# Kernel tuning notes

Hardware: AMD Instinct MI355X
Metric: run time of the kernel (lower is better)

Reference implementation:

```python
import jax, jax.numpy as jnp
import numpy as np

QD = 512        # query_dim == key_dim
SD = 64         # spa_embed_dim
K = 4           # num_attn heads
EPS = 1e-6      # LayerNorm eps (space2vec LayerNorm)
SLOPE = 0.01    # nn.LeakyReLU default negative_slope


def setup_inputs() -> dict:
    key = jax.random.key(0)
    ks = jax.random.split(key, 6)
    B, N = 4096, 32
    D = 2 * QD + SD  # concat dim when have_query_embed=True
    xav = (6.0 / (D + K)) ** 0.5
    return {
        "key_embeds": jax.random.normal(ks[0], (B, N, QD), dtype=jnp.float32),
        "key_spa_embeds": jax.random.normal(ks[1], (B, N, SD), dtype=jnp.float32),
        "query_embed": jax.random.normal(ks[2], (B, QD), dtype=jnp.float32),
        "atten_vecs": jax.random.uniform(ks[3], (D, K), minval=-xav, maxval=xav, dtype=jnp.float32),
        "post_w": jax.random.normal(ks[4], (QD, QD), dtype=jnp.float32) * 0.02,
        "post_b": jnp.zeros((QD,), dtype=jnp.float32),
        "pre_ln_g": jnp.ones((QD,), dtype=jnp.float32),
        "pre_ln_b": jnp.zeros((QD,), dtype=jnp.float32),
        "post_ln_g": jnp.ones((QD,), dtype=jnp.float32),
        "post_ln_b": jnp.zeros((QD,), dtype=jnp.float32),
    }


def _layernorm(x, g, b):
    m = jnp.mean(x, axis=-1, keepdims=True)
    v = jnp.mean((x - m) ** 2, axis=-1, keepdims=True)
    return g * (x - m) / jnp.sqrt(v + EPS) + b


def reference(key_embeds, key_spa_embeds, query_embed, atten_vecs,
              post_w, post_b, pre_ln_g, pre_ln_b, post_ln_g, post_ln_b):
    B, N, _ = key_embeds.shape
    # expand query over context points and concat: [B, N, 2*QD+SD]
    q_exp = jnp.broadcast_to(query_embed[:, None, :], (B, N, QD))
    concat = jnp.concatenate([q_exp, key_embeds, key_spa_embeds], axis=2)
    # attention logits per head: [B, N, K]
    attn = jnp.einsum('bnd,dk->bnk', concat, atten_vecs)
    attn = jax.nn.leaky_relu(attn, SLOPE)
    attn = jax.nn.softmax(attn, axis=1)  # softmax over context points
    # weighted sum per head, then average over heads: [B, QD]
    combined = jnp.einsum('bnk,bnd->bkd', attn, key_embeds).sum(axis=1) * (1.0 / K)
    combined = jax.nn.sigmoid(combined)
    # pre layernorm with residual from query
    combined = _layernorm(combined + query_embed, pre_ln_g, pre_ln_b)
    # post linear (dropout in eval mode = identity) + residual + post LN
    lin = combined @ post_w.T + post_b
    out = _layernorm(lin + combined, post_ln_g, post_ln_b)
    return out
```

## Files before the change

kernel.cpp:

```cpp
#include <hip/hip_runtime.h>
#include <hip/hip_bf16.h>

#define QD 512
#define SD 64
#define NCTX 32
#define KTOT 576
#define ROWB 1152

constexpr float EPS_LN = 1e-6f;
constexpr float SLOPE = 0.01f;

typedef __attribute__((ext_vector_type(8))) __bf16 bf16x8;
typedef __attribute__((ext_vector_type(4))) float f32x4;

__device__ __forceinline__ float red64(float v) {
#pragma unroll
    for (int m = 32; m; m >>= 1) v += __shfl_xor(v, m, 64);
    return v;
}

__device__ __forceinline__ float b2f(unsigned short u) {
    unsigned int x = ((unsigned int)u) << 16;
    return __builtin_bit_cast(float, x);
}

__device__ __forceinline__ int swz(int row, int off) {
    return row * ROWB + (off ^ ((row & 7) << 4));
}

__device__ __forceinline__ bf16x8 pack8(float4 a, float4 b) {
    bf16x8 r;
    r[0] = (__bf16)a.x; r[1] = (__bf16)a.y; r[2] = (__bf16)a.z; r[3] = (__bf16)a.w;
    r[4] = (__bf16)b.x; r[5] = (__bf16)b.y; r[6] = (__bf16)b.z; r[7] = (__bf16)b.w;
    return r;
}

__global__ __launch_bounds__(256, 3) void attn_fuse(
    const float* __restrict__ key, const float* __restrict__ spa,
    const float* __restrict__ query, const float* __restrict__ av,
    const float* __restrict__ lng, const float* __restrict__ lnb,
    float* __restrict__ yout)
{
    __shared__ __align__(16) unsigned char s_A[NCTX * ROWB];
    __shared__ __align__(16) unsigned char s_B[4 * ROWB];
    __shared__ float s_logit[NCTX][4];
    __shared__ float s_w[NCTX];
    __shared__ float s_red[8];
    __shared__ float s_ql[4];

    const int b = blockIdx.x;
    const int t = threadIdx.x;
    const int wave = t >> 6;
    const int lane = t & 63;

    const float* kb = key + (size_t)b * (NCTX * QD);
    const float* qb = query + (size_t)b * QD;
    const float* sb = spa + (size_t)b * (NCTX * SD);
    const float4* av4 = reinterpret_cast<const float4*>(av);

    float4 kreg[16];
#pragma unroll
    for (int i = 0; i < 8; ++i) {
        const float* krow = kb + (8 * wave + i) * QD;
        kreg[2 * i]     = reinterpret_cast<const float4*>(krow)[2 * lane];
        kreg[2 * i + 1] = reinterpret_cast<const float4*>(krow)[2 * lane + 1];
    }
    const int i2 = lane >> 3, j8 = lane & 7;
    const float* srow = sb + (8 * wave + i2) * SD + 8 * j8;
    const float4 sreg0 = reinterpret_cast<const float4*>(srow)[0];
    const float4 sreg1 = reinterpret_cast<const float4*>(srow)[1];
    float avreg[9];
#pragma unroll
    for (int r = 0; r < 9; ++r)
        avreg[r] = av[(size_t)(512 + lane * 9 + r) * 4 + wave];

#pragma unroll
    for (int i = 0; i < 8; ++i) {
        const int n = 8 * wave + i;
        *reinterpret_cast<bf16x8*>(&s_A[swz(n, 16 * lane)]) =
            pack8(kreg[2 * i], kreg[2 * i + 1]);
    }
    *reinterpret_cast<bf16x8*>(&s_A[swz(8 * wave + i2, 1024 + 16 * j8)]) =
        pack8(sreg0, sreg1);
#pragma unroll
    for (int r = 0; r < 9; ++r) {
        const int k = lane * 9 + r;
        *reinterpret_cast<__bf16*>(&s_B[wave * ROWB + ((2 * k) ^ (wave << 4))]) =
            (__bf16)avreg[r];
    }

    if (wave == 3) {
        const float4* q4 = reinterpret_cast<const float4*>(qb);
        float s0 = 0.f, s1 = 0.f, s2 = 0.f, s3 = 0.f;
#pragma unroll
        for (int h = 0; h < 2; ++h) {
            const float4 qv = q4[2 * lane + h];
            const float4 a0 = av4[8 * lane + 4 * h + 0];
            const float4 a1 = av4[8 * lane + 4 * h + 1];
            const float4 a2 = av4[8 * lane + 4 * h + 2];
            const float4 a3 = av4[8 * lane + 4 * h + 3];
            s0 += qv.x * a0.x + qv.y * a1.x + qv.z * a2.x + qv.w * a3.x;
            s1 += qv.x * a0.y + qv.y * a1.y + qv.z * a2.y + qv.w * a3.y;
            s2 += qv.x * a0.z + qv.y * a1.z + qv.z * a2.z + qv.w * a3.z;
            s3 += qv.x * a0.w + qv.y * a1.w + qv.z * a2.w + qv.w * a3.w;
        }
        s0 = red64(s0); s1 = red64(s1); s2 = red64(s2); s3 = red64(s3);
        if (lane == 0) { s_ql[0] = s0; s_ql[1] = s1; s_ql[2] = s2; s_ql[3] = s3; }
    }
    __syncthreads();

    if (wave < 2) {
        const int colB = lane & 15;
        const int kgrp = (lane >> 4) * 16;
        const int arow = 16 * wave + (lane & 15);
        f32x4 acc = {0.f, 0.f, 0.f, 0.f};
        bf16x8 bz;
#pragma unroll
        for (int e = 0; e < 8; ++e) bz[e] = (__bf16)0.0f;
#pragma unroll
        for (int ks = 0; ks < 18; ++ks) {
            const int koff = ks * 64 + kgrp;
            const bf16x8 af =
                *reinterpret_cast<const bf16x8*>(&s_A[swz(arow, koff)]);
            bf16x8 bf = bz;
            if (colB < 4)
                bf = *reinterpret_cast<const bf16x8*>(
                    &s_B[colB * ROWB + (koff ^ (colB << 4))]);
            acc = __builtin_amdgcn_mfma_f32_16x16x32_bf16(af, bf, acc, 0, 0, 0);
        }
        if (colB < 4) {
            const float qlk = s_ql[colB];
#pragma unroll
            for (int r = 0; r < 4; ++r) {
                const int row = 16 * wave + (lane >> 4) * 4 + r;
                float v = acc[r] + qlk;
                v = v > 0.f ? v : SLOPE * v;
                s_logit[row][colB] = v;
            }
        }
    }
    __syncthreads();

    if (wave == 0) {
        const int n = lane & 31;
        float v0 = s_logit[n][0], v1 = s_logit[n][1],
              v2 = s_logit[n][2], v3 = s_logit[n][3];
        float m0 = v0, m1 = v1, m2 = v2, m3 = v3;
#pragma unroll
        for (int m = 16; m; m >>= 1) {
            m0 = fmaxf(m0, __shfl_xor(m0, m, 32));
            m1 = fmaxf(m1, __shfl_xor(m1, m, 32));
            m2 = fmaxf(m2, __shfl_xor(m2, m, 32));
            m3 = fmaxf(m3, __shfl_xor(m3, m, 32));
        }
        float e0 = __expf(v0 - m0), e1 = __expf(v1 - m1),
              e2 = __expf(v2 - m2), e3 = __expf(v3 - m3);
        float st0 = e0, st1 = e1, st2 = e2, st3 = e3;
#pragma unroll
        for (int m = 16; m; m >>= 1) {
            st0 += __shfl_xor(st0, m, 32);
            st1 += __shfl_xor(st1, m, 32);
            st2 += __shfl_xor(st2, m, 32);
            st3 += __shfl_xor(st3, m, 32);
        }
        const float w = 0.25f * (e0 / st0 + e1 / st1 + e2 / st2 + e3 / st3);
        if (lane < 32) s_w[n] = w;
    }
    __syncthreads();

    const int d0 = 2 * t;
    float acc0 = 0.f, acc1 = 0.f;
#pragma unroll
    for (int n = 0; n < NCTX; ++n) {
        const float wn = s_w[n];
        const unsigned int u =
            *reinterpret_cast<const unsigned int*>(&s_A[swz(n, 4 * t)]);
        acc0 += wn * b2f((unsigned short)(u & 0xffffu));
        acc1 += wn * b2f((unsigned short)(u >> 16));
    }
    const float2 qv = *reinterpret_cast<const float2*>(&qb[d0]);
    const float x0 = 1.f / (1.f + __expf(-acc0)) + qv.x;
    const float x1 = 1.f / (1.f + __expf(-acc1)) + qv.y;

    float sum = red64(x0 + x1);
    float ssq = red64(x0 * x0 + x1 * x1);
    if (lane == 0) { s_red[wave] = sum; s_red[4 + wave] = ssq; }
    __syncthreads();
    sum = s_red[0] + s_red[1] + s_red[2] + s_red[3];
    ssq = s_red[4] + s_red[5] + s_red[6] + s_red[7];
    const float mean = sum * (1.f / QD);
    const float var = ssq * (1.f / QD) - mean * mean;
    const float inv = rsqrtf(var + EPS_LN);
    const float2 gg = *reinterpret_cast<const float2*>(&lng[d0]);
    const float2 bb = *reinterpret_cast<const float2*>(&lnb[d0]);
    float2 o;
    o.x = gg.x * (x0 - mean) * inv + bb.x;
    o.y = gg.y * (x1 - mean) * inv + bb.y;
    *reinterpret_cast<float2*>(&yout[(size_t)b * QD + d0]) = o;
}

__device__ __forceinline__ int swzB(int row, int off) {
    return row * 128 + (off ^ ((row & 7) << 4));
}

__global__ __launch_bounds__(256) void post_gemm(
    const float* __restrict__ Y, const float* __restrict__ W,
    const float* __restrict__ pbias, float* __restrict__ out)
{
    __shared__ __align__(16) unsigned char Ys[64 * 128];
    __shared__ __align__(16) unsigned char Ws[64 * 128];
    const int t = threadIdx.x;
    const int wave = t >> 6, lane = t & 63;
    const int bm = blockIdx.x * 64;
    const int bn = blockIdx.y * 64;

    const int lr = t >> 2;
    const int lq = (t & 3) * 16;

    f32x4 acc[4] = {{0.f,0.f,0.f,0.f},{0.f,0.f,0.f,0.f},
                    {0.f,0.f,0.f,0.f},{0.f,0.f,0.f,0.f}};

    for (int kc = 0; kc < QD; kc += 64) {
        float4 ya[4], wa[4];
        const float* yrow = Y + (size_t)(bm + lr) * QD + kc + lq;
        const float* wrow = W + (size_t)(bn + lr) * QD + kc + lq;
#pragma unroll
        for (int j = 0; j < 4; ++j) {
            ya[j] = reinterpret_cast<const float4*>(yrow)[j];
            wa[j] = reinterpret_cast<const float4*>(wrow)[j];
        }
        __syncthreads();
        const int base = lq * 2;
        *reinterpret_cast<bf16x8*>(&Ys[swzB(lr, base)])      = pack8(ya[0], ya[1]);
        *reinterpret_cast<bf16x8*>(&Ys[swzB(lr, base + 16)]) = pack8(ya[2], ya[3]);
        *reinterpret_cast<bf16x8*>(&Ws[swzB(lr, base)])      = pack8(wa[0], wa[1]);
        *reinterpret_cast<bf16x8*>(&Ws[swzB(lr, base + 16)]) = pack8(wa[2], wa[3]);
        __syncthreads();
#pragma unroll
        for (int ks = 0; ks < 2; ++ks) {
            const int ko = ks * 64 + (lane >> 4) * 16;
            const bf16x8 af = *reinterpret_cast<const bf16x8*>(
                &Ys[swzB(16 * wave + (lane & 15), ko)]);
#pragma unroll
            for (int c = 0; c < 4; ++c) {
                const bf16x8 bf = *reinterpret_cast<const bf16x8*>(
                    &Ws[swzB(16 * c + (lane & 15), ko)]);
                acc[c] = __builtin_amdgcn_mfma_f32_16x16x32_bf16(af, bf, acc[c],
                                                                 0, 0, 0);
            }
        }
    }
    const int m0 = bm + 16 * wave + (lane >> 4) * 4;
#pragma unroll
    for (int c = 0; c < 4; ++c) {
        const int n = bn + 16 * c + (lane & 15);
        const float pb = pbias[n];
#pragma unroll
        for (int r = 0; r < 4; ++r) {
            out[(size_t)(m0 + r) * QD + n] = acc[c][r] + pb;
        }
    }
}

__global__ __launch_bounds__(256) void post_ln_kernel(
    float* __restrict__ out, const float* __restrict__ yres,
    const float* __restrict__ lng, const float* __restrict__ lnb)
{
    __shared__ float s_red[8];
    const int r = blockIdx.x;
    const int t = threadIdx.x;
    const int wave = t >> 6, lane = t & 63;
    const int d0 = 2 * t;
    const float2 lv = *reinterpret_cast<const float2*>(&out[(size_t)r * QD + d0]);
    const float2 yv = *reinterpret_cast<const float2*>(&yres[(size_t)r * QD + d0]);
    const float x0 = lv.x + yv.x;
    const float x1 = lv.y + yv.y;
    float sum = red64(x0 + x1);
    float ssq = red64(x0 * x0 + x1 * x1);
    if (lane == 0) { s_red[wave] = sum; s_red[4 + wave] = ssq; }
    __syncthreads();
    sum = s_red[0] + s_red[1] + s_red[2] + s_red[3];
    ssq = s_red[4] + s_red[5] + s_red[6] + s_red[7];
    const float mean = sum * (1.f / QD);
    const float var = ssq * (1.f / QD) - mean * mean;
    const float inv = rsqrtf(var + EPS_LN);
    const float2 gg = *reinterpret_cast<const float2*>(&lng[d0]);
    const float2 bb = *reinterpret_cast<const float2*>(&lnb[d0]);
    float2 o;
    o.x = gg.x * (x0 - mean) * inv + bb.x;
    o.y = gg.y * (x1 - mean) * inv + bb.y;
    *reinterpret_cast<float2*>(&out[(size_t)r * QD + d0]) = o;
}

extern "C" void kernel_launch(void* const* d_in, const int* in_sizes, int n_in,
                              void* d_out, int out_size, void* d_ws, size_t ws_size,
                              hipStream_t stream) {
    const float* key    = (const float*)d_in[0];
    const float* spa    = (const float*)d_in[1];
    const float* query  = (const float*)d_in[2];
    const float* av     = (const float*)d_in[3];
    const float* postw  = (const float*)d_in[4];
    const float* postb  = (const float*)d_in[5];
    const float* pre_g  = (const float*)d_in[6];
    const float* pre_b  = (const float*)d_in[7];
    const float* post_g = (const float*)d_in[8];
    const float* post_b = (const float*)d_in[9];
    float* out = (float*)d_out;
    float* yws = (float*)d_ws;

    const int B = in_sizes[2] / QD;

    attn_fuse<<<B, 256, 0, stream>>>(key, spa, query, av, pre_g, pre_b, yws);
    dim3 gridB(B / 64, QD / 64);
    post_gemm<<<gridB, 256, 0, stream>>>(yws, postw, postb, out);
    post_ln_kernel<<<B, 256, 0, stream>>>(out, yws, post_g, post_b);
}
```

Before: 85.37 us.

## Split key staging into two passes, drop s_B, compute logits in every wave

Stages the key rows into shared memory in two half-passes so fewer registers stay live, and raises the launch-bounds occupancy target from 3 to 4 blocks per CU. Removes the attention-vector shared buffer and the query-logit shared slot. Every wave now computes the query logit redundantly and runs its own small MFMA over its 8 rows, with the attention vectors loaded straight from global memory as the A operand. This drops one barrier and the idle waves, at the cost of redundant global reads of atten_vecs in every wave and a more serialized load-then-store of the keys.

```diff
diff --git a/kernel.cpp b/kernel.cpp
--- a/kernel.cpp
+++ b/kernel.cpp
@@ -35,18 +35,16 @@
     return r;
 }
 
-__global__ __launch_bounds__(256, 3) void attn_fuse(
+__global__ __launch_bounds__(256, 4) void attn_fuse(
     const float* __restrict__ key, const float* __restrict__ spa,
     const float* __restrict__ query, const float* __restrict__ av,
     const float* __restrict__ lng, const float* __restrict__ lnb,
     float* __restrict__ yout)
 {
     __shared__ __align__(16) unsigned char s_A[NCTX * ROWB];
-    __shared__ __align__(16) unsigned char s_B[4 * ROWB];
     __shared__ float s_logit[NCTX][4];
     __shared__ float s_w[NCTX];
     __shared__ float s_red[8];
-    __shared__ float s_ql[4];
 
     const int b = blockIdx.x;
     const int t = threadIdx.x;
@@ -58,40 +56,34 @@
     const float* sb = spa + (size_t)b * (NCTX * SD);
     const float4* av4 = reinterpret_cast<const float4*>(av);
 
-    float4 kreg[16];
-#pragma unroll
-    for (int i = 0; i < 8; ++i) {
-        const float* krow = kb + (8 * wave + i) * QD;
-        kreg[2 * i]     = reinterpret_cast<const float4*>(krow)[2 * lane];
-        kreg[2 * i + 1] = reinterpret_cast<const float4*>(krow)[2 * lane + 1];
-    }
-    const int i2 = lane >> 3, j8 = lane & 7;
-    const float* srow = sb + (8 * wave + i2) * SD + 8 * j8;
-    const float4 sreg0 = reinterpret_cast<const float4*>(srow)[0];
-    const float4 sreg1 = reinterpret_cast<const float4*>(srow)[1];
-    float avreg[9];
-#pragma unroll
-    for (int r = 0; r < 9; ++r)
-        avreg[r] = av[(size_t)(512 + lane * 9 + r) * 4 + wave];
-
-#pragma unroll
-    for (int i = 0; i < 8; ++i) {
-        const int n = 8 * wave + i;
-        *reinterpret_cast<bf16x8*>(&s_A[swz(n, 16 * lane)]) =
-            pack8(kreg[2 * i], kreg[2 * i + 1]);
-    }
-    *reinterpret_cast<bf16x8*>(&s_A[swz(8 * wave + i2, 1024 + 16 * j8)]) =
-        pack8(sreg0, sreg1);
-#pragma unroll
-    for (int r = 0; r < 9; ++r) {
-        const int k = lane * 9 + r;
-        *reinterpret_cast<__bf16*>(&s_B[wave * ROWB + ((2 * k) ^ (wave << 4))]) =
-            (__bf16)avreg[r];
-    }
-
-    if (wave == 3) {
+#pragma unroll
+    for (int pass = 0; pass < 2; ++pass) {
+        float4 kr[8];
+#pragma unroll
+        for (int i = 0; i < 4; ++i) {
+            const float* krow = kb + (8 * wave + 4 * pass + i) * QD;
+            kr[2 * i]     = reinterpret_cast<const float4*>(krow)[2 * lane];
+            kr[2 * i + 1] = reinterpret_cast<const float4*>(krow)[2 * lane + 1];
+        }
+#pragma unroll
+        for (int i = 0; i < 4; ++i) {
+            const int n = 8 * wave + 4 * pass + i;
+            *reinterpret_cast<bf16x8*>(&s_A[swz(n, 16 * lane)]) =
+                pack8(kr[2 * i], kr[2 * i + 1]);
+        }
+    }
+    {
+        const int i2 = lane >> 3, j8 = lane & 7;
+        const float* srow = sb + (8 * wave + i2) * SD + 8 * j8;
+        const float4 s0 = reinterpret_cast<const float4*>(srow)[0];
+        const float4 s1 = reinterpret_cast<const float4*>(srow)[1];
+        *reinterpret_cast<bf16x8*>(&s_A[swz(8 * wave + i2, 1024 + 16 * j8)]) =
+            pack8(s0, s1);
+    }
+
+    float ql0 = 0.f, ql1 = 0.f, ql2 = 0.f, ql3 = 0.f;
+    {
         const float4* q4 = reinterpret_cast<const float4*>(qb);
-        float s0 = 0.f, s1 = 0.f, s2 = 0.f, s3 = 0.f;
 #pragma unroll
         for (int h = 0; h < 2; ++h) {
             const float4 qv = q4[2 * lane + h];
@@ -99,44 +91,46 @@
             const float4 a1 = av4[8 * lane + 4 * h + 1];
             const float4 a2 = av4[8 * lane + 4 * h + 2];
             const float4 a3 = av4[8 * lane + 4 * h + 3];
-            s0 += qv.x * a0.x + qv.y * a1.x + qv.z * a2.x + qv.w * a3.x;
-            s1 += qv.x * a0.y + qv.y * a1.y + qv.z * a2.y + qv.w * a3.y;
-            s2 += qv.x * a0.z + qv.y * a1.z + qv.z * a2.z + qv.w * a3.z;
-            s3 += qv.x * a0.w + qv.y * a1.w + qv.z * a2.w + qv.w * a3.w;
-        }
-        s0 = red64(s0); s1 = red64(s1); s2 = red64(s2); s3 = red64(s3);
-        if (lane == 0) { s_ql[0] = s0; s_ql[1] = s1; s_ql[2] = s2; s_ql[3] = s3; }
-    }
-    __syncthreads();
-
-    if (wave < 2) {
-        const int colB = lane & 15;
-        const int kgrp = (lane >> 4) * 16;
-        const int arow = 16 * wave + (lane & 15);
+            ql0 += qv.x * a0.x + qv.y * a1.x + qv.z * a2.x + qv.w * a3.x;
+            ql1 += qv.x * a0.y + qv.y * a1.y + qv.z * a2.y + qv.w * a3.y;
+            ql2 += qv.x * a0.z + qv.y * a1.z + qv.z * a2.z + qv.w * a3.z;
+            ql3 += qv.x * a0.w + qv.y * a1.w + qv.z * a2.w + qv.w * a3.w;
+        }
+        ql0 = red64(ql0); ql1 = red64(ql1); ql2 = red64(ql2); ql3 = red64(ql3);
+    }
+
+    {
+        const int qq = lane >> 4;
+        const int c15 = lane & 15;
+        const int brow = 8 * wave + (c15 & 7);
         f32x4 acc = {0.f, 0.f, 0.f, 0.f};
         bf16x8 bz;
 #pragma unroll
         for (int e = 0; e < 8; ++e) bz[e] = (__bf16)0.0f;
 #pragma unroll
         for (int ks = 0; ks < 18; ++ks) {
-            const int koff = ks * 64 + kgrp;
-            const bf16x8 af =
-                *reinterpret_cast<const bf16x8*>(&s_A[swz(arow, koff)]);
-            bf16x8 bf = bz;
-            if (colB < 4)
-                bf = *reinterpret_cast<const bf16x8*>(
-                    &s_B[colB * ROWB + (koff ^ (colB << 4))]);
-            acc = __builtin_amdgcn_mfma_f32_16x16x32_bf16(af, bf, acc, 0, 0, 0);
-        }
-        if (colB < 4) {
-            const float qlk = s_ql[colB];
-#pragma unroll
-            for (int r = 0; r < 4; ++r) {
-                const int row = 16 * wave + (lane >> 4) * 4 + r;
-                float v = acc[r] + qlk;
-                v = v > 0.f ? v : SLOPE * v;
-                s_logit[row][colB] = v;
+            const int koff = ks * 64 + qq * 16;
+            const bf16x8 xb =
+                *reinterpret_cast<const bf16x8*>(&s_A[swz(brow, koff)]);
+            bf16x8 af = bz;
+            if (c15 < 4) {
+                const float* ap = av + (size_t)(512 + ks * 32 + qq * 8) * 4 + c15;
+#pragma unroll
+                for (int j = 0; j < 8; ++j) af[j] = (__bf16)ap[4 * j];
             }
+            acc = __builtin_amdgcn_mfma_f32_16x16x32_bf16(af, xb, acc, 0, 0, 0);
+        }
+        if (lane < 8) {
+            float l0 = acc[0] + ql0, l1 = acc[1] + ql1,
+                  l2 = acc[2] + ql2, l3 = acc[3] + ql3;
+            l0 = l0 > 0.f ? l0 : SLOPE * l0;
+            l1 = l1 > 0.f ? l1 : SLOPE * l1;
+            l2 = l2 > 0.f ? l2 : SLOPE * l2;
+            l3 = l3 > 0.f ? l3 : SLOPE * l3;
+            s_logit[8 * wave + lane][0] = l0;
+            s_logit[8 * wave + lane][1] = l1;
+            s_logit[8 * wave + lane][2] = l2;
+            s_logit[8 * wave + lane][3] = l3;
         }
     }
     __syncthreads();
```

Result: slower. 101.8 us (+19.2%).

## Shrink LDS rows, feed spatial MFMA operands from registers, raise occupancy

Applied to the files above, without the earlier changes.

The spatial-embedding part of the logits GEMM is now loaded straight into registers by the two MFMA waves, not staged in shared memory, so each shared row shrinks from 1152 to 1088 bytes and the XOR swizzle is dropped. Key rows are loaded in two passes of four rows to lower peak register use, and launch bounds ask for 4 blocks per CU instead of 3. The aim is higher occupancy to hide global-load latency. The risk is more LDS bank conflicts with the padded unswizzled layout, and less load-level parallelism per wave.

```diff
diff --git a/kernel.cpp b/kernel.cpp
--- a/kernel.cpp
+++ b/kernel.cpp
@@ -4,7 +4,7 @@
 #define QD 512
 #define SD 64
 #define NCTX 32
-#define KTOT 576
+#define ROWA 1088
 #define ROWB 1152
 
 constexpr float EPS_LN = 1e-6f;
@@ -22,10 +22,6 @@
 __device__ __forceinline__ float b2f(unsigned short u) {
     unsigned int x = ((unsigned int)u) << 16;
     return __builtin_bit_cast(float, x);
-}
-
-__device__ __forceinline__ int swz(int row, int off) {
-    return row * ROWB + (off ^ ((row & 7) << 4));
 }
 
 __device__ __forceinline__ bf16x8 pack8(float4 a, float4 b) {
@@ -35,13 +31,13 @@
     return r;
 }
 
-__global__ __launch_bounds__(256, 3) void attn_fuse(
+__global__ __launch_bounds__(256, 4) void attn_fuse(
     const float* __restrict__ key, const float* __restrict__ spa,
     const float* __restrict__ query, const float* __restrict__ av,
     const float* __restrict__ lng, const float* __restrict__ lnb,
     float* __restrict__ yout)
 {
-    __shared__ __align__(16) unsigned char s_A[NCTX * ROWB];
+    __shared__ __align__(16) unsigned char s_A[NCTX * ROWA];
     __shared__ __align__(16) unsigned char s_B[4 * ROWB];
     __shared__ float s_logit[NCTX][4];
     __shared__ float s_w[NCTX];
@@ -58,30 +54,37 @@
     const float* sb = spa + (size_t)b * (NCTX * SD);
     const float4* av4 = reinterpret_cast<const float4*>(av);
 
-    float4 kreg[16];
-#pragma unroll
-    for (int i = 0; i < 8; ++i) {
-        const float* krow = kb + (8 * wave + i) * QD;
-        kreg[2 * i]     = reinterpret_cast<const float4*>(krow)[2 * lane];
-        kreg[2 * i + 1] = reinterpret_cast<const float4*>(krow)[2 * lane + 1];
-    }
-    const int i2 = lane >> 3, j8 = lane & 7;
-    const float* srow = sb + (8 * wave + i2) * SD + 8 * j8;
-    const float4 sreg0 = reinterpret_cast<const float4*>(srow)[0];
-    const float4 sreg1 = reinterpret_cast<const float4*>(srow)[1];
+#pragma unroll
+    for (int pass = 0; pass < 2; ++pass) {
+        float4 kr[8];
+#pragma unroll
+        for (int i = 0; i < 4; ++i) {
+            const float* krow = kb + (8 * wave + 4 * pass + i) * QD;
+            kr[2 * i]     = reinterpret_cast<const float4*>(krow)[2 * lane];
+            kr[2 * i + 1] = reinterpret_cast<const float4*>(krow)[2 * lane + 1];
+        }
+#pragma unroll
+        for (int i = 0; i < 4; ++i) {
+            const int n = 8 * wave + 4 * pass + i;
+            *reinterpret_cast<bf16x8*>(&s_A[n * ROWA + 16 * lane]) =
+                pack8(kr[2 * i], kr[2 * i + 1]);
+        }
+    }
+    float4 sp0a, sp0b, sp1a, sp1b;
+    if (wave < 2) {
+        const int arow = 16 * wave + (lane & 15);
+        const int qq8 = (lane >> 4) * 8;
+        const float* s0p = sb + arow * SD + qq8;
+        const float* s1p = sb + arow * SD + 32 + qq8;
+        sp0a = reinterpret_cast<const float4*>(s0p)[0];
+        sp0b = reinterpret_cast<const float4*>(s0p)[1];
+        sp1a = reinterpret_cast<const float4*>(s1p)[0];
+        sp1b = reinterpret_cast<const float4*>(s1p)[1];
+    }
     float avreg[9];
 #pragma unroll
     for (int r = 0; r < 9; ++r)
         avreg[r] = av[(size_t)(512 + lane * 9 + r) * 4 + wave];
-
-#pragma unroll
-    for (int i = 0; i < 8; ++i) {
-        const int n = 8 * wave + i;
-        *reinterpret_cast<bf16x8*>(&s_A[swz(n, 16 * lane)]) =
-            pack8(kreg[2 * i], kreg[2 * i + 1]);
-    }
-    *reinterpret_cast<bf16x8*>(&s_A[swz(8 * wave + i2, 1024 + 16 * j8)]) =
-        pack8(sreg0, sreg1);
 #pragma unroll
     for (int r = 0; r < 9; ++r) {
         const int k = lane * 9 + r;
@@ -118,10 +121,20 @@
 #pragma unroll
         for (int e = 0; e < 8; ++e) bz[e] = (__bf16)0.0f;
 #pragma unroll
-        for (int ks = 0; ks < 18; ++ks) {
+        for (int ks = 0; ks < 16; ++ks) {
             const int koff = ks * 64 + kgrp;
             const bf16x8 af =
-                *reinterpret_cast<const bf16x8*>(&s_A[swz(arow, koff)]);
+                *reinterpret_cast<const bf16x8*>(&s_A[arow * ROWA + koff]);
+            bf16x8 bf = bz;
+            if (colB < 4)
+                bf = *reinterpret_cast<const bf16x8*>(
+                    &s_B[colB * ROWB + (koff ^ (colB << 4))]);
+            acc = __builtin_amdgcn_mfma_f32_16x16x32_bf16(af, bf, acc, 0, 0, 0);
+        }
+#pragma unroll
+        for (int ks = 0; ks < 2; ++ks) {
+            const int koff = 1024 + ks * 64 + kgrp;
+            const bf16x8 af = (ks == 0) ? pack8(sp0a, sp0b) : pack8(sp1a, sp1b);
             bf16x8 bf = bz;
             if (colB < 4)
                 bf = *reinterpret_cast<const bf16x8*>(
@@ -174,7 +187,7 @@
     for (int n = 0; n < NCTX; ++n) {
         const float wn = s_w[n];
         const unsigned int u =
-            *reinterpret_cast<const unsigned int*>(&s_A[swz(n, 4 * t)]);
+            *reinterpret_cast<const unsigned int*>(&s_A[n * ROWA + 4 * t]);
         acc0 += wn * b2f((unsigned short)(u & 0xffffu));
         acc1 += wn * b2f((unsigned short)(u >> 16));
     }
```

Result: faster. 82.19 us (-3.7%).
